# Kernel tuning notes

Measured on AMD Instinct MI355X. Metric: run time of the kernel, lower is better.

The kernel has to match this reference:

```python
import jax, jax.numpy as jnp
import numpy as np

VOCAB = 32000
EMB = 512
HID = 1024
OUT = 2

def setup_inputs() -> dict:
    key = jax.random.key(0)
    ks = jax.random.split(key, 8)
    stdv = 1.0 / np.sqrt(HID)
    x = jax.random.randint(ks[0], (512, 128), 0, VOCAB)
    emb = jax.random.normal(ks[1], (VOCAB, EMB), dtype=jnp.float32)
    w_ih = jax.random.uniform(ks[2], (4 * HID, EMB), minval=-stdv, maxval=stdv, dtype=jnp.float32)
    w_hh = jax.random.uniform(ks[3], (4 * HID, HID), minval=-stdv, maxval=stdv, dtype=jnp.float32)
    b_ih = jax.random.uniform(ks[4], (4 * HID,), minval=-stdv, maxval=stdv, dtype=jnp.float32)
    b_hh = jax.random.uniform(ks[5], (4 * HID,), minval=-stdv, maxval=stdv, dtype=jnp.float32)
    fc_w = jax.random.normal(ks[6], (OUT, HID), dtype=jnp.float32) * 0.02
    fc_b = jnp.zeros((OUT,), dtype=jnp.float32)
    return {"x": x, "emb": emb, "w_ih": w_ih, "w_hh": w_hh,
            "b_ih": b_ih, "b_hh": b_hh, "fc_w": fc_w, "fc_b": fc_b}

def reference(x, emb, w_ih, w_hh, b_ih, b_hh, fc_w, fc_b):
    T, B = x.shape
    embedded = emb[x]  # [T, B, EMB]
    # precompute input projections for all steps: [T, B, 4H]
    x_gates = jnp.einsum('tbe,ge->tbg', embedded, w_ih) + b_ih + b_hh
    h0 = jnp.zeros((B, HID), dtype=embedded.dtype)
    c0 = jnp.zeros((B, HID), dtype=embedded.dtype)

    def step(carry, xg):
        hx, cx = carry
        gates = xg + hx @ w_hh.T  # [B, 4H]
        i, f, g, o = jnp.split(gates, 4, axis=1)
        i = jax.nn.sigmoid(i)
        f = jax.nn.sigmoid(f)
        g = jnp.tanh(g)
        o = jax.nn.sigmoid(o)
        cy = f * cx + i * g
        hy = o * jnp.tanh(cy)
        return (hy, cy), hy

    (hT, cT), all_h = jax.lax.scan(step, (h0, c0), x_gates)
    out = hT @ fc_w.T + fc_b  # [B, OUT]
    return out
```

## Files before the change

### kernel.cpp

```cpp
#include <hip/hip_runtime.h>

typedef short short8 __attribute__((ext_vector_type(8)));
typedef float f32x4 __attribute__((ext_vector_type(4)));
typedef unsigned int u32x4 __attribute__((ext_vector_type(4)));
typedef unsigned int u32x2 __attribute__((ext_vector_type(2)));

#define T_STEPS 512
#define BATCH   128
#define EMBD    512
#define HID     1024
#define NWG     256
#define NTHR    1024
#define NGROUP  8
#define WPG     32

#define SLOT_STRIDE 16
#define SLOT_BYTES  (NWG * SLOT_STRIDE * 4)
#define GR_OFF    SLOT_BYTES
#define GR_BYTES  1024
#define H_OFF     (SLOT_BYTES + GR_BYTES)
#define H_BYTES   (NGROUP * 2 * 32768)
#define WH_OFF    (H_OFF + H_BYTES)
#define WH_BYTES  (32u*32u*8u*64u*8u*2u)
#define WI_OFF    (WH_OFF + WH_BYTES)
#define WI_BYTES  (32u*16u*8u*64u*8u*2u)
#define BS_OFF    (WI_OFF + WI_BYTES)
#define BS_BYTES  (4096 * 4)
#define PT_OFF    (BS_OFF + BS_BYTES)
#define PT_BYTES  (BATCH * 32 * 2 * 4)
#define EMB_OFF   (PT_OFF + PT_BYTES)
#define EMB_BYTES ((size_t)T_STEPS*16*8*64*8*2)
#define WS_NEEDED (EMB_OFF + EMB_BYTES)

__device__ __forceinline__ unsigned short f2b(float f) {
    unsigned u = __builtin_bit_cast(unsigned, f);
    u += 0x7FFFu + ((u >> 16) & 1u);
    return (unsigned short)(u >> 16);
}

__device__ __forceinline__ uint4 pack8(float4 a, float4 b) {
    uint4 r;
    r.x = (unsigned)f2b(a.x) | ((unsigned)f2b(a.y) << 16);
    r.y = (unsigned)f2b(a.z) | ((unsigned)f2b(a.w) << 16);
    r.z = (unsigned)f2b(b.x) | ((unsigned)f2b(b.y) << 16);
    r.w = (unsigned)f2b(b.z) | ((unsigned)f2b(b.w) << 16);
    return r;
}

__device__ __forceinline__ float fsig(float x) {
    float e = __expf(-fabsf(x));
    float r = 1.f / (1.f + e);
    return x >= 0.f ? r : 1.f - r;
}
__device__ __forceinline__ float ftanh_(float x) {
    float e = __expf(-2.f * fabsf(x));
    float r = (1.f - e) / (1.f + e);
    return x >= 0.f ? r : -r;
}

__device__ __forceinline__ void llc_load16(const void* p, u32x4& v) {
    asm volatile("global_load_dwordx4 %0, %1, off sc0 sc1" : "=v"(v) : "v"(p));
}
__device__ __forceinline__ void llc_store8(void* p, u32x2 v) {
    asm volatile("global_store_dwordx2 %0, %1, off sc0 sc1" :: "v"(p), "v"(v) : "memory");
}
__device__ __forceinline__ void waitvm0() {
    asm volatile("s_waitcnt vmcnt(0)" ::: "memory");
}

__global__ void prep_wh(const float* __restrict__ w_hh, unsigned short* __restrict__ wh_arr) {
    int gid = blockIdx.x * blockDim.x + threadIdx.x;
    int l  = gid & 63;
    int nq = (gid >> 6) & 7;
    int ks = (gid >> 9) & 31;
    int w  = gid >> 14;
    int lr = nq * 16 + (l & 15);
    int grow = (lr >> 5) * HID + w * 32 + (lr & 31);
    int k = ks * 32 + (l >> 4) * 8;
    const float4* src = reinterpret_cast<const float4*>(w_hh + (size_t)grow * HID + k);
    *reinterpret_cast<uint4*>(wh_arr + (size_t)gid * 8) = pack8(src[0], src[1]);
}

__global__ void prep_wi(const float* __restrict__ w_ih, unsigned short* __restrict__ wi_arr) {
    int gid = blockIdx.x * blockDim.x + threadIdx.x;
    int l  = gid & 63;
    int nq = (gid >> 6) & 7;
    int eks = (gid >> 9) & 15;
    int w  = gid >> 13;
    int lr = nq * 16 + (l & 15);
    int grow = (lr >> 5) * HID + w * 32 + (lr & 31);
    int k = eks * 32 + (l >> 4) * 8;
    const float4* src = reinterpret_cast<const float4*>(w_ih + (size_t)grow * EMBD + k);
    *reinterpret_cast<uint4*>(wi_arr + (size_t)gid * 8) = pack8(src[0], src[1]);
}

__global__ void prep_bsum(const float* __restrict__ b_ih, const float* __restrict__ b_hh,
                          float* __restrict__ bs) {
    int gid = blockIdx.x * blockDim.x + threadIdx.x;
    int w = gid >> 7, lr = gid & 127;
    int grow = (lr >> 5) * HID + w * 32 + (lr & 31);
    bs[gid] = b_ih[grow] + b_hh[grow];
}

__global__ void prep_emb(const int* __restrict__ x, const float* __restrict__ emb,
                         unsigned short* __restrict__ emb_arr) {
    int gid = blockIdx.x * blockDim.x + threadIdx.x;
    int l  = gid & 63;
    int mt = (gid >> 6) & 7;
    int ks = (gid >> 9) & 15;
    int t  = gid >> 13;
    int b  = mt * 16 + (l & 15);
    int k  = ks * 32 + (l >> 4) * 8;
    int tok = x[t * BATCH + b];
    const float4* src = reinterpret_cast<const float4*>(emb + (size_t)tok * EMBD + k);
    *reinterpret_cast<uint4*>(emb_arr + (size_t)gid * 8) = pack8(src[0], src[1]);
}

__global__ __launch_bounds__(NTHR) void lstm_main(
    const unsigned short* __restrict__ wh_arr,
    const unsigned short* __restrict__ wi_arr,
    const float* __restrict__ bs_arr,
    const unsigned short* __restrict__ emb_arr,
    unsigned short* __restrict__ h_arr,
    const float* __restrict__ fc_w,
    float* __restrict__ partials,
    unsigned* __restrict__ slots)
{
    __shared__ __align__(16) unsigned short wis[16 * 8 * 64 * 8];
    __shared__ __align__(16) char ovl[32768];
    float* gbf    = reinterpret_cast<float*>(ovl);
    u32x4* stage4 = reinterpret_cast<u32x4*>(ovl);
    unsigned short* stage = reinterpret_cast<unsigned short*>(ovl);

    unsigned* gr = slots + (GR_OFF >> 2);

    const int tid  = threadIdx.x;
    const int wgid = blockIdx.x;
    const int g = wgid >> 5;
    const int w = wgid & 31;

    {
        const uint4* s2 = reinterpret_cast<const uint4*>(wi_arr + (size_t)w * 65536);
        uint4* d2 = reinterpret_cast<uint4*>(wis);
        for (int i = tid; i < 8192; i += NTHR) d2[i] = s2[i];
    }

    const int lane = tid & 63;
    const int wave = tid >> 6;
    const int nq   = wave >> 1;
    const int kq   = wave & 1;

    short8 bh[16];
    #pragma unroll
    for (int s = 0; s < 16; ++s) {
        int ks = kq * 16 + s;
        bh[s] = *reinterpret_cast<const short8*>(wh_arr + (size_t)(((w * 32 + ks) * 8 + nq) * 64 + lane) * 8);
    }

    const int lrD   = nq * 16 + (lane & 15);
    const int rbase = (lane >> 4) * 4;
    const float bini = (kq == 0) ? bs_arr[w * 128 + lrD] : 0.f;

    const int pb = tid & 15;
    const int qd = tid >> 4;
    float cs[4] = {0.f, 0.f, 0.f, 0.f};
    float hr[4] = {0.f, 0.f, 0.f, 0.f};

    __syncthreads();

    for (int t = 0; t < T_STEPS; ++t) {
        f32x4 acc = {bini, bini, bini, bini};

        const unsigned short* ebuf = emb_arr + (size_t)t * 65536;
        #pragma unroll
        for (int s = 0; s < 8; ++s) {
            int eks = kq * 8 + s;
            short8 a  = *reinterpret_cast<const short8*>(ebuf + ((eks * 8 + g) * 64 + lane) * 8);
            short8 bw = *reinterpret_cast<const short8*>(wis + ((eks * 8 + nq) * 64 + lane) * 8);
            acc = __builtin_amdgcn_mfma_f32_16x16x32_bf16(a, bw, acc, 0, 0, 0);
        }

        if (t > 0) {
            if (w == 0) {
                if (tid < WPG) {
                    while (__hip_atomic_load(&slots[(g * WPG + tid) * SLOT_STRIDE],
                                             __ATOMIC_RELAXED, __HIP_MEMORY_SCOPE_AGENT) < (unsigned)t) {}
                }
                asm volatile("" ::: "memory");
                if (tid == 0)
                    __hip_atomic_store(&gr[g * 32], (unsigned)t,
                                       __ATOMIC_RELAXED, __HIP_MEMORY_SCOPE_AGENT);
            } else {
                if (tid == 0) {
                    while (__hip_atomic_load(&gr[g * 32],
                                             __ATOMIC_RELAXED, __HIP_MEMORY_SCOPE_AGENT) < (unsigned)t) {}
                }
            }
            __syncthreads();

            const char* hb = reinterpret_cast<const char*>(h_arr) + (size_t)(g * 2 + (t & 1)) * 32768;
            u32x4 v0, v1;
            llc_load16(hb + tid * 16, v0);
            llc_load16(hb + (tid + 1024) * 16, v1);
            waitvm0();
            __builtin_amdgcn_sched_barrier(0);
            stage4[tid] = v0;
            stage4[tid + 1024] = v1;
            __syncthreads();

            #pragma unroll
            for (int s = 0; s < 16; ++s) {
                int ks = kq * 16 + s;
                short8 a = *reinterpret_cast<const short8*>(stage + (ks * 64 + lane) * 8);
                acc = __builtin_amdgcn_mfma_f32_16x16x32_bf16(a, bh[s], acc, 0, 0, 0);
            }
        }
        __syncthreads();

        #pragma unroll
        for (int jj = 0; jj < 4; ++jj)
            gbf[kq * 2112 + (rbase + jj) * 132 + lrD] = acc[jj];
        __syncthreads();

        if (tid < 128) {
            const float* g0 = gbf + pb * 132;
            const float* g1 = gbf + 2112 + pb * 132;
            const int cb = qd * 4;
            float4 xi = *reinterpret_cast<const float4*>(g0 + cb);
            float4 xf = *reinterpret_cast<const float4*>(g0 + 32 + cb);
            float4 xg = *reinterpret_cast<const float4*>(g0 + 64 + cb);
            float4 xo = *reinterpret_cast<const float4*>(g0 + 96 + cb);
            float4 yi = *reinterpret_cast<const float4*>(g1 + cb);
            float4 yf = *reinterpret_cast<const float4*>(g1 + 32 + cb);
            float4 yg = *reinterpret_cast<const float4*>(g1 + 64 + cb);
            float4 yo = *reinterpret_cast<const float4*>(g1 + 96 + cb);
            float ti[4] = {xi.x + yi.x, xi.y + yi.y, xi.z + yi.z, xi.w + yi.w};
            float tf[4] = {xf.x + yf.x, xf.y + yf.y, xf.z + yf.z, xf.w + yf.w};
            float tg[4] = {xg.x + yg.x, xg.y + yg.y, xg.z + yg.z, xg.w + yg.w};
            float to[4] = {xo.x + yo.x, xo.y + yo.y, xo.z + yo.z, xo.w + yo.w};
            #pragma unroll
            for (int e = 0; e < 4; ++e) {
                float ig = fsig(ti[e]), fg = fsig(tf[e]), gg = ftanh_(tg[e]), og = fsig(to[e]);
                cs[e] = fg * cs[e] + ig * gg;
                hr[e] = og * ftanh_(cs[e]);
            }
            u32x2 pk;
            pk.x = (unsigned)f2b(hr[0]) | ((unsigned)f2b(hr[1]) << 16);
            pk.y = (unsigned)f2b(hr[2]) | ((unsigned)f2b(hr[3]) << 16);
            char* hd = reinterpret_cast<char*>(h_arr) + (size_t)(g * 2 + ((t + 1) & 1)) * 32768;
            llc_store8(hd + (w * 64 + (qd >> 1) * 16 + pb) * 16 + (qd & 1) * 8, pk);
            waitvm0();
        }
        __syncthreads();
        if (tid == 0) {
            __hip_atomic_store(&slots[(g * WPG + w) * SLOT_STRIDE], (unsigned)(t + 1),
                               __ATOMIC_RELAXED, __HIP_MEMORY_SCOPE_AGENT);
        }
    }

    __syncthreads();
    float* red = reinterpret_cast<float*>(ovl);
    if (tid < 128) {
        float v0 = 0.f, v1 = 0.f;
        #pragma unroll
        for (int e = 0; e < 4; ++e) {
            int col = w * 32 + qd * 4 + e;
            v0 += hr[e] * fc_w[col];
            v1 += hr[e] * fc_w[HID + col];
        }
        red[tid * 2]     = v0;
        red[tid * 2 + 1] = v1;
    }
    __syncthreads();
    if (tid < 32) {
        int b = tid >> 1, o = tid & 1;
        float s = 0.f;
        for (int q = 0; q < 8; ++q) s += red[((q << 4) | b) * 2 + o];
        partials[((g * 16 + b) * 32 + w) * 2 + o] = s;
    }
}

__global__ void finalize(const float* __restrict__ partials, const float* __restrict__ fc_b,
                         float* __restrict__ out) {
    int tid = threadIdx.x;
    int b = tid >> 1, o = tid & 1;
    float s = fc_b[o];
    for (int w = 0; w < 32; ++w) s += partials[(b * 32 + w) * 2 + o];
    out[b * 2 + o] = s;
}

extern "C" void kernel_launch(void* const* d_in, const int* in_sizes, int n_in,
                              void* d_out, int out_size, void* d_ws, size_t ws_size,
                              hipStream_t stream) {
    const int*   x    = (const int*)d_in[0];
    const float* emb  = (const float*)d_in[1];
    const float* w_ih = (const float*)d_in[2];
    const float* w_hh = (const float*)d_in[3];
    const float* b_ih = (const float*)d_in[4];
    const float* b_hh = (const float*)d_in[5];
    const float* fc_w = (const float*)d_in[6];
    const float* fc_b = (const float*)d_in[7];
    float* out = (float*)d_out;
    char* ws = (char*)d_ws;

    if (ws_size < WS_NEEDED) {
        (void)hipMemsetAsync(d_out, 0xFF, (size_t)out_size * sizeof(float), stream);
        return;
    }

    unsigned*       slots   = (unsigned*)(ws);
    unsigned short* h_arr   = (unsigned short*)(ws + H_OFF);
    unsigned short* wh_arr  = (unsigned short*)(ws + WH_OFF);
    unsigned short* wi_arr  = (unsigned short*)(ws + WI_OFF);
    float*          bs_arr  = (float*)(ws + BS_OFF);
    float*          pt_arr  = (float*)(ws + PT_OFF);
    unsigned short* emb_arr = (unsigned short*)(ws + EMB_OFF);

    (void)hipMemsetAsync(ws, 0, SLOT_BYTES + GR_BYTES, stream);

    prep_wh  <<<2048, 256, 0, stream>>>(w_hh, wh_arr);
    prep_wi  <<<1024, 256, 0, stream>>>(w_ih, wi_arr);
    prep_bsum<<<16,   256, 0, stream>>>(b_ih, b_hh, bs_arr);
    prep_emb <<<16384,256, 0, stream>>>(x, emb, emb_arr);
    lstm_main<<<NWG, NTHR, 0, stream>>>(wh_arr, wi_arr, bs_arr, emb_arr, h_arr,
                                        fc_w, pt_arr, slots);
    finalize <<<1, 256, 0, stream>>>(pt_arr, fc_b, out);
}
```

Measured before the change: 3.858 ms.

## Replace two-level group barrier with per-wave flags polled by one wave

Swaps the hierarchical barrier (leader workgroup gathers 32 slots, then broadcasts a group flag) for a flat one. Each of the two writer waves publishes its own flag right after its h store, one wave in every workgroup polls all 64 group flags, and the trailing __syncthreads is dropped. The h loads are now issued before the input-projection MFMAs so their latency overlaps that compute, which removes a sync hop per step. It adds a poll cap that can break out early on a timeout, which would silently read stale h, and more flag traffic to the LLC.

```diff
diff --git a/kernel.cpp b/kernel.cpp
--- a/kernel.cpp
+++ b/kernel.cpp
@@ -14,11 +14,8 @@
 #define NGROUP  8
 #define WPG     32
 
-#define SLOT_STRIDE 16
-#define SLOT_BYTES  (NWG * SLOT_STRIDE * 4)
-#define GR_OFF    SLOT_BYTES
-#define GR_BYTES  1024
-#define H_OFF     (SLOT_BYTES + GR_BYTES)
+#define CTRL_BYTES 4096
+#define H_OFF     CTRL_BYTES
 #define H_BYTES   (NGROUP * 2 * 32768)
 #define WH_OFF    (H_OFF + H_BYTES)
 #define WH_BYTES  (32u*32u*8u*64u*8u*2u)
@@ -32,6 +29,8 @@
 #define EMB_BYTES ((size_t)T_STEPS*16*8*64*8*2)
 #define WS_NEEDED (EMB_OFF + EMB_BYTES)
 
+#define POLL_CAP  (1u << 17)
+
 __device__ __forceinline__ unsigned short f2b(float f) {
     unsigned u = __builtin_bit_cast(unsigned, f);
     u += 0x7FFFu + ((u >> 16) & 1u);
@@ -61,8 +60,17 @@
 __device__ __forceinline__ void llc_load16(const void* p, u32x4& v) {
     asm volatile("global_load_dwordx4 %0, %1, off sc0 sc1" : "=v"(v) : "v"(p));
 }
+__device__ __forceinline__ unsigned llc_load4(const void* p) {
+    unsigned v;
+    asm volatile("global_load_dword %0, %1, off sc0 sc1\n\ts_waitcnt vmcnt(0)"
+                 : "=v"(v) : "v"(p) : "memory");
+    return v;
+}
 __device__ __forceinline__ void llc_store8(void* p, u32x2 v) {
     asm volatile("global_store_dwordx2 %0, %1, off sc0 sc1" :: "v"(p), "v"(v) : "memory");
+}
+__device__ __forceinline__ void llc_store4(void* p, unsigned v) {
+    asm volatile("global_store_dword %0, %1, off sc0 sc1" :: "v"(p), "v"(v) : "memory");
 }
 __device__ __forceinline__ void waitvm0() {
     asm volatile("s_waitcnt vmcnt(0)" ::: "memory");
@@ -124,7 +132,7 @@
     unsigned short* __restrict__ h_arr,
     const float* __restrict__ fc_w,
     float* __restrict__ partials,
-    unsigned* __restrict__ slots)
+    unsigned* __restrict__ ctrl)
 {
     __shared__ __align__(16) unsigned short wis[16 * 8 * 64 * 8];
     __shared__ __align__(16) char ovl[32768];
@@ -132,12 +140,11 @@
     u32x4* stage4 = reinterpret_cast<u32x4*>(ovl);
     unsigned short* stage = reinterpret_cast<unsigned short*>(ovl);
 
-    unsigned* gr = slots + (GR_OFF >> 2);
-
-    const int tid  = threadIdx.x;
-    const int wgid = blockIdx.x;
-    const int g = wgid >> 5;
-    const int w = wgid & 31;
+    unsigned* flags = ctrl + 64;
+
+    const int tid = threadIdx.x;
+    const int g = (int)(blockIdx.x >> 5);
+    const int w = (int)(blockIdx.x & 31);
 
     {
         const uint4* s2 = reinterpret_cast<const uint4*>(wi_arr + (size_t)w * 65536);
@@ -169,7 +176,27 @@
     __syncthreads();
 
     for (int t = 0; t < T_STEPS; ++t) {
+        const unsigned tu = (unsigned)t;
         f32x4 acc = {bini, bini, bini, bini};
+        u32x4 v0, v1;
+
+        if (t > 0) {
+            if (wave == 15) {
+                const unsigned* fl = flags + g * 64 + lane;
+                unsigned spins = 0;
+                for (;;) {
+                    unsigned v = llc_load4(fl);
+                    if (__all((int)(v >= tu))) break;
+                    if (++spins > POLL_CAP) break;
+                    asm volatile("s_sleep 1");
+                }
+            }
+            __syncthreads();
+
+            const char* hb = reinterpret_cast<const char*>(h_arr) + (size_t)(g * 2 + (t & 1)) * 32768;
+            llc_load16(hb + tid * 16, v0);
+            llc_load16(hb + (tid + 1024) * 16, v1);
+        }
 
         const unsigned short* ebuf = emb_arr + (size_t)t * 65536;
         #pragma unroll
@@ -181,27 +208,6 @@
         }
 
         if (t > 0) {
-            if (w == 0) {
-                if (tid < WPG) {
-                    while (__hip_atomic_load(&slots[(g * WPG + tid) * SLOT_STRIDE],
-                                             __ATOMIC_RELAXED, __HIP_MEMORY_SCOPE_AGENT) < (unsigned)t) {}
-                }
-                asm volatile("" ::: "memory");
-                if (tid == 0)
-                    __hip_atomic_store(&gr[g * 32], (unsigned)t,
-                                       __ATOMIC_RELAXED, __HIP_MEMORY_SCOPE_AGENT);
-            } else {
-                if (tid == 0) {
-                    while (__hip_atomic_load(&gr[g * 32],
-                                             __ATOMIC_RELAXED, __HIP_MEMORY_SCOPE_AGENT) < (unsigned)t) {}
-                }
-            }
-            __syncthreads();
-
-            const char* hb = reinterpret_cast<const char*>(h_arr) + (size_t)(g * 2 + (t & 1)) * 32768;
-            u32x4 v0, v1;
-            llc_load16(hb + tid * 16, v0);
-            llc_load16(hb + (tid + 1024) * 16, v1);
             waitvm0();
             __builtin_amdgcn_sched_barrier(0);
             stage4[tid] = v0;
@@ -250,26 +256,24 @@
             char* hd = reinterpret_cast<char*>(h_arr) + (size_t)(g * 2 + ((t + 1) & 1)) * 32768;
             llc_store8(hd + (w * 64 + (qd >> 1) * 16 + pb) * 16 + (qd & 1) * 8, pk);
             waitvm0();
-        }
-        __syncthreads();
-        if (tid == 0) {
-            __hip_atomic_store(&slots[(g * WPG + w) * SLOT_STRIDE], (unsigned)(t + 1),
-                               __ATOMIC_RELAXED, __HIP_MEMORY_SCOPE_AGENT);
+            if ((tid & 63) == 0) {
+                llc_store4(flags + g * 64 + w * 2 + (tid >> 6), tu + 1u);
+            }
         }
     }
 
     __syncthreads();
     float* red = reinterpret_cast<float*>(ovl);
     if (tid < 128) {
-        float v0 = 0.f, v1 = 0.f;
+        float v0f = 0.f, v1f = 0.f;
         #pragma unroll
         for (int e = 0; e < 4; ++e) {
             int col = w * 32 + qd * 4 + e;
-            v0 += hr[e] * fc_w[col];
-            v1 += hr[e] * fc_w[HID + col];
-        }
-        red[tid * 2]     = v0;
-        red[tid * 2 + 1] = v1;
+            v0f += hr[e] * fc_w[col];
+            v1f += hr[e] * fc_w[HID + col];
+        }
+        red[tid * 2]     = v0f;
+        red[tid * 2 + 1] = v1f;
     }
     __syncthreads();
     if (tid < 32) {
@@ -308,7 +312,7 @@
         return;
     }
 
-    unsigned*       slots   = (unsigned*)(ws);
+    unsigned*       ctrl    = (unsigned*)(ws);
     unsigned short* h_arr   = (unsigned short*)(ws + H_OFF);
     unsigned short* wh_arr  = (unsigned short*)(ws + WH_OFF);
     unsigned short* wi_arr  = (unsigned short*)(ws + WI_OFF);
@@ -316,13 +320,13 @@
     float*          pt_arr  = (float*)(ws + PT_OFF);
     unsigned short* emb_arr = (unsigned short*)(ws + EMB_OFF);
 
-    (void)hipMemsetAsync(ws, 0, SLOT_BYTES + GR_BYTES, stream);
+    (void)hipMemsetAsync(ws, 0, CTRL_BYTES, stream);
 
     prep_wh  <<<2048, 256, 0, stream>>>(w_hh, wh_arr);
     prep_wi  <<<1024, 256, 0, stream>>>(w_ih, wi_arr);
     prep_bsum<<<16,   256, 0, stream>>>(b_ih, b_hh, bs_arr);
     prep_emb <<<16384,256, 0, stream>>>(x, emb, emb_arr);
     lstm_main<<<NWG, NTHR, 0, stream>>>(wh_arr, wi_arr, bs_arr, emb_arr, h_arr,
-                                        fc_w, pt_arr, slots);
+                                        fc_w, pt_arr, ctrl);
     finalize <<<1, 256, 0, stream>>>(pt_arr, fc_b, out);
 }
```

After: 6.033 ms. 1.56x slower.
